# Kernel optimization log

Measured on AMD Instinct MI355X. Metric: run time of the kernel, lower is better.

Reference implementation:

```python
import jax, jax.numpy as jnp
import numpy as np

N_NODES = 50000
N_EDGES = 800000
D_IN = 64
D_HID = 64
N_LAYERS = 3
BN_EPS = 1e-5


def setup_inputs() -> dict:
    key = jax.random.key(0)
    ks = jax.random.split(key, 10)
    x = jax.random.normal(ks[0], (N_NODES, D_IN), dtype=jnp.float32)
    edge_index = jax.random.randint(ks[1], (2, N_EDGES), 0, N_NODES, dtype=jnp.int32)
    # Per-layer GCN weights (in==hid==64 so we can stack) and BatchNorm params.
    Ws = jax.random.normal(ks[2], (N_LAYERS, D_HID, D_HID), dtype=jnp.float32) / np.sqrt(D_HID)
    bs = jnp.zeros((N_LAYERS, D_HID), dtype=jnp.float32)
    gammas = jnp.ones((N_LAYERS, D_HID), dtype=jnp.float32)
    betas = jnp.zeros((N_LAYERS, D_HID), dtype=jnp.float32)
    means = jax.random.normal(ks[3], (N_LAYERS, D_HID), dtype=jnp.float32) * 0.1
    variances = jax.random.uniform(ks[4], (N_LAYERS, D_HID), dtype=jnp.float32, minval=0.5, maxval=1.5)
    lin_w = jax.random.normal(ks[5], (D_HID, 1), dtype=jnp.float32) / np.sqrt(D_HID)
    lin_b = jnp.zeros((1,), dtype=jnp.float32)
    return {"x": x, "edge_index": edge_index, "Ws": Ws, "bs": bs,
            "gammas": gammas, "betas": betas, "means": means,
            "variances": variances, "lin_w": lin_w, "lin_b": lin_b}


def _gnn_forward(x, edge_index, Ws, bs, gammas, betas, means, variances, lin_w, lin_b):
    n = x.shape[0]
    # GCNConv: add self loops, symmetric D^{-1/2}(A+I)D^{-1/2} normalization.
    loop = jnp.arange(n, dtype=edge_index.dtype)
    row = jnp.concatenate([edge_index[0], loop])  # source nodes
    col = jnp.concatenate([edge_index[1], loop])  # target nodes
    deg = jax.ops.segment_sum(jnp.ones(row.shape[0], x.dtype), col, num_segments=n)
    dinv = jax.lax.rsqrt(jnp.maximum(deg, 1.0))  # deg >= 1 from self loops
    norm = (dinv[row] * dinv[col])[:, None]  # [E+N, 1]

    h = x
    for i in range(N_LAYERS):
        h = h @ Ws[i]  # transform first (PyG GCNConv order)
        h = jax.ops.segment_sum(h[row] * norm, col, num_segments=n) + bs[i]
        # BatchNorm1d (eval mode: running stats) + ReLU; dropout is identity in eval.
        h = (h - means[i]) * jax.lax.rsqrt(variances[i] + BN_EPS) * gammas[i] + betas[i]
        h = jax.nn.relu(h)
    out = h @ lin_w + lin_b  # [N, 1]
    return out[:, 0]


def reference(x, edge_index, Ws, bs, gammas, betas, means, variances, lin_w, lin_b):
    return _gnn_forward(x, edge_index, Ws, bs, gammas, betas, means, variances, lin_w, lin_b)
```

## Files before the change

### kernel.cpp

```cpp
#include <hip/hip_runtime.h>
#include <hip/hip_bf16.h>
#include <hip/hip_fp16.h>


#define BN_EPS 1e-5f
#define CAP 64
#define CHUNK 2048
#define BINSH 7
#define SEGCAP 2560
#define NBINS_MAX 512

typedef _Float16 f16x8 __attribute__((ext_vector_type(8)));
typedef float f32x4 __attribute__((ext_vector_type(4)));

__global__ __launch_bounds__(256) void k_bin_pairs(const int* __restrict__ row,
                                                   const int* __restrict__ col,
                                                   int* __restrict__ gfill,
                                                   unsigned int* __restrict__ gpairs,
                                                   int e, int nbins) {
    __shared__ unsigned int pl[CHUNK];
    __shared__ int bcnt[NBINS_MAX];
    __shared__ int bbase[NBINS_MAX];
    int tid = threadIdx.x;
    int base = blockIdx.x * CHUNK;
    for (int b = tid; b < nbins; b += 256) bcnt[b] = 0;
    __syncthreads();
    int nloc = e - base; if (nloc > CHUNK) nloc = CHUNK;
    #pragma unroll
    for (int it = 0; it < CHUNK / 1024; ++it) {
        int le = (it * 256 + tid) * 4;
        if (le + 3 < nloc) {
            int i4 = (base >> 2) + it * 256 + tid;
            int4 r = ((const int4*)row)[i4];
            int4 c = ((const int4*)col)[i4];
            atomicAdd(&bcnt[c.x >> BINSH], 1); pl[le + 0] = (unsigned)r.x | ((unsigned)c.x << 16);
            atomicAdd(&bcnt[c.y >> BINSH], 1); pl[le + 1] = (unsigned)r.y | ((unsigned)c.y << 16);
            atomicAdd(&bcnt[c.z >> BINSH], 1); pl[le + 2] = (unsigned)r.z | ((unsigned)c.z << 16);
            atomicAdd(&bcnt[c.w >> BINSH], 1); pl[le + 3] = (unsigned)r.w | ((unsigned)c.w << 16);
        } else {
            for (int j = 0; j < 4; ++j) {
                if (le + j < nloc) {
                    int rr = row[base + le + j];
                    int cc = col[base + le + j];
                    atomicAdd(&bcnt[cc >> BINSH], 1);
                    pl[le + j] = (unsigned)rr | ((unsigned)cc << 16);
                }
            }
        }
    }
    __syncthreads();
    for (int b = tid; b < nbins; b += 256) {
        int cb = bcnt[b];
        bbase[b] = cb ? atomicAdd(&gfill[b], cb) : 0;
        bcnt[b] = 0;
    }
    __syncthreads();
    for (int i = tid; i < nloc; i += 256) {
        unsigned int p = pl[i];
        int bin = p >> (16 + BINSH);
        int off = atomicAdd(&bcnt[bin], 1);
        int pos = bbase[bin] + off;
        if (pos < SEGCAP) gpairs[(size_t)bin * SEGCAP + pos] = p;
    }
}

__global__ __launch_bounds__(256) void k_bucket_build(const unsigned int* __restrict__ gpairs,
                                                      const int* __restrict__ gfill,
                                                      int* __restrict__ cnt,
                                                      unsigned short* __restrict__ bucket,
                                                      const float* __restrict__ Ws,
                                                      __half* __restrict__ wt,
                                                      int n) {
    __shared__ unsigned short lb[128 * CAP];
    __shared__ int lc[128];
    int tid = threadIdx.x;
    int bin = blockIdx.x;
    if (tid < 128) lc[tid] = 0;
    __syncthreads();
    int m = gfill[bin]; if (m > SEGCAP) m = SEGCAP;
    const unsigned int* seg = gpairs + (size_t)bin * SEGCAP;
    for (int i = tid; i < m; i += 256) {
        unsigned int p = seg[i];
        int src = p & 0xffff;
        int dl = (p >> 16) & 127;
        int pos = atomicAdd(&lc[dl], 1);
        if (pos < CAP) lb[dl * CAP + pos] = (unsigned short)src;
    }
    __syncthreads();
    int nodebase = bin << BINSH;
    const int4* lb4 = (const int4*)lb;
    int4* gb4 = (int4*)bucket;
    for (int i = tid; i < 128 * 8; i += 256) {
        int rrow = i >> 3;
        int gnode = nodebase + rrow;
        if (gnode < n) gb4[(size_t)gnode * 8 + (i & 7)] = lb4[i];
    }
    if (tid < 128) {
        int gnode = nodebase + tid;
        if (gnode < n) cnt[gnode] = lc[tid];
    }
    if (bin < 3) {
        const float* W = Ws + bin * 4096;
        __half* hi = wt + (size_t)bin * 8192;
        __half* lo = hi + 4096;
        for (int i = tid; i < 4096; i += 256) {
            int k = i >> 6, nn = i & 63;
            float w = W[k * 64 + nn];
            __half h = __float2half_rn(w);
            hi[nn * 64 + k] = h;
            lo[nn * 64 + k] = __float2half_rn(w - __half2float(h));
        }
    }
}

template<bool L0>
__global__ __launch_bounds__(256) void k_mm_mfma(const void* __restrict__ Ain,
                                                 const __half* __restrict__ wt,
                                                 const int* __restrict__ cnt,
                                                 __half* __restrict__ out, int n) {
    int tid = threadIdx.x;
    int w = tid >> 6;
    int lane = tid & 63;
    int r = lane & 15;
    int kg = lane >> 4;
    int row = blockIdx.x * 64 + w * 16 + r;
    bool inb = row < n;

    f16x8 ahi0 = {}, ahi1 = {}, alo0 = {}, alo1 = {};
    if (L0) {
        const float* A = (const float*)Ain;
        if (inb) {
            float di = rsqrtf((float)(cnt[row] + 1));
            const float4* ap0 = (const float4*)(A + (size_t)row * 64 + kg * 8);
            const float4* ap1 = (const float4*)(A + (size_t)row * 64 + 32 + kg * 8);
            float4 v0 = ap0[0], v1 = ap0[1];
            float4 v2 = ap1[0], v3 = ap1[1];
            float f[16] = {v0.x, v0.y, v0.z, v0.w, v1.x, v1.y, v1.z, v1.w,
                           v2.x, v2.y, v2.z, v2.w, v3.x, v3.y, v3.z, v3.w};
            #pragma unroll
            for (int i = 0; i < 8; ++i) {
                float s0 = f[i] * di, s1 = f[8 + i] * di;
                _Float16 h0 = (_Float16)s0, h1 = (_Float16)s1;
                ahi0[i] = h0; ahi1[i] = h1;
                alo0[i] = (_Float16)(s0 - (float)h0);
                alo1[i] = (_Float16)(s1 - (float)h1);
            }
        }
    } else {
        const __half* A = (const __half*)Ain;
        if (inb) {
            union { uint4 u; f16x8 h; } u0, u1;
            u0.u = *(const uint4*)(A + (size_t)row * 64 + kg * 8);
            u1.u = *(const uint4*)(A + (size_t)row * 64 + 32 + kg * 8);
            ahi0 = u0.h; ahi1 = u1.h;
        }
    }

    const __half* whi = wt;
    const __half* wlo = wt + 4096;
    f32x4 acc[4];
    #pragma unroll
    for (int t = 0; t < 4; ++t) {
        int cb = t * 16 + r;
        union { uint4 u; f16x8 h; } bh0, bh1, bl0, bl1;
        bh0.u = *(const uint4*)(whi + cb * 64 + kg * 8);
        bh1.u = *(const uint4*)(whi + cb * 64 + 32 + kg * 8);
        bl0.u = *(const uint4*)(wlo + cb * 64 + kg * 8);
        bl1.u = *(const uint4*)(wlo + cb * 64 + 32 + kg * 8);
        f32x4 a = {0.f, 0.f, 0.f, 0.f};
        a = __builtin_amdgcn_mfma_f32_16x16x32_f16(ahi0, bh0.h, a, 0, 0, 0);
        a = __builtin_amdgcn_mfma_f32_16x16x32_f16(ahi1, bh1.h, a, 0, 0, 0);
        a = __builtin_amdgcn_mfma_f32_16x16x32_f16(ahi0, bl0.h, a, 0, 0, 0);
        a = __builtin_amdgcn_mfma_f32_16x16x32_f16(ahi1, bl1.h, a, 0, 0, 0);
        if (L0) {
            a = __builtin_amdgcn_mfma_f32_16x16x32_f16(alo0, bh0.h, a, 0, 0, 0);
            a = __builtin_amdgcn_mfma_f32_16x16x32_f16(alo1, bh1.h, a, 0, 0, 0);
        }
        acc[t] = a;
    }

    int orow_base = blockIdx.x * 64 + w * 16 + 4 * kg;
    #pragma unroll
    for (int t = 0; t < 4; ++t) {
        #pragma unroll
        for (int i = 0; i < 4; ++i) {
            int orow = orow_base + i;
            if (orow < n) out[(size_t)orow * 64 + t * 16 + r] = __float2half_rn(acc[t][i]);
        }
    }
}

template<int LAYER, bool FINAL>
__global__ __launch_bounds__(256, 6) void k_agg(const __half* __restrict__ t,
                                                const int* __restrict__ cnt,
                                                const unsigned short* __restrict__ bucket,
                                                const float* __restrict__ bias,
                                                const float* __restrict__ gamma,
                                                const float* __restrict__ beta,
                                                const float* __restrict__ mean,
                                                const float* __restrict__ var,
                                                __half* __restrict__ hout,
                                                const float* __restrict__ lw,
                                                const float* __restrict__ lb,
                                                float* __restrict__ outp, int n) {
    int lane = threadIdx.x & 63;
    int g = lane >> 3;
    int q = lane & 7;
    int qo = q << 3;
    float S[8], O[8], LW[8];
    #pragma unroll
    for (int i = 0; i < 8; ++i) {
        int f = qo + i;
        float s = gamma[f] * rsqrtf(var[f] + BN_EPS);
        S[i] = s;
        O[i] = fmaf(bias[f] - mean[f], s, beta[f]);
        if (FINAL) LW[i] = lw[f];
    }
    int wave = (blockIdx.x * blockDim.x + threadIdx.x) >> 6;
    int nwaves = (gridDim.x * blockDim.x) >> 6;
    union HV { float4 f4; __half2 h2[4]; };
    int node = wave;
    int c_pf = 0, idx_pf = 0;
    if (node < n) {
        c_pf = cnt[node];
        idx_pf = (int)bucket[(size_t)node * CAP + lane];
    }
    for (; node < n; node += nwaves) {
        int c = c_pf;
        int myidx = idx_pf;
        HV vself;
        vself.f4 = *(const float4*)(t + ((size_t)node << 6) + qo);
        int nn = node + nwaves;
        if (nn < n) {
            c_pf = cnt[nn];
            idx_pf = (int)bucket[(size_t)nn * CAP + lane];
        }
        int cm1 = c - 1; if (cm1 < 0) cm1 = 0;
        int i1 = __shfl(myidx, (g < cm1 ? g : cm1), 64);
        int i2 = __shfl(myidx, (8 + g < cm1 ? 8 + g : cm1), 64);
        HV v1, v2, v3, v4;
        v1.f4 = *(const float4*)(t + ((size_t)i1 << 6) + qo);
        v2.f4 = *(const float4*)(t + ((size_t)i2 << 6) + qo);
        if (c > 16) {
            int i3 = __shfl(myidx, (16 + g < cm1 ? 16 + g : cm1), 64);
            int i4 = __shfl(myidx, (24 + g < cm1 ? 24 + g : cm1), 64);
            v3.f4 = *(const float4*)(t + ((size_t)i3 << 6) + qo);
            v4.f4 = *(const float4*)(t + ((size_t)i4 << 6) + qo);
        }
        float acc[8] = {0.f, 0.f, 0.f, 0.f, 0.f, 0.f, 0.f, 0.f};
        for (int sub = 0; sub < c; sub += 32) {
            float m1 = (sub + g < c) ? 1.f : 0.f;
            float m2 = (sub + 8 + g < c) ? 1.f : 0.f;
            #pragma unroll
            for (int p = 0; p < 4; ++p) {
                float2 a = __half22float2(v1.h2[p]);
                float2 b = __half22float2(v2.h2[p]);
                acc[2 * p]     = fmaf(m1, a.x, acc[2 * p]);
                acc[2 * p + 1] = fmaf(m1, a.y, acc[2 * p + 1]);
                acc[2 * p]     = fmaf(m2, b.x, acc[2 * p]);
                acc[2 * p + 1] = fmaf(m2, b.y, acc[2 * p + 1]);
            }
            if (sub + 32 < c) {
                int t1 = sub + 32 + g, t2 = sub + 40 + g;
                i1 = __shfl(myidx, (t1 < cm1 ? t1 : cm1), 64);
                i2 = __shfl(myidx, (t2 < cm1 ? t2 : cm1), 64);
                v1.f4 = *(const float4*)(t + ((size_t)i1 << 6) + qo);
                v2.f4 = *(const float4*)(t + ((size_t)i2 << 6) + qo);
            }
            if (sub + 16 < c) {
                float m3 = (sub + 16 + g < c) ? 1.f : 0.f;
                float m4 = (sub + 24 + g < c) ? 1.f : 0.f;
                #pragma unroll
                for (int p = 0; p < 4; ++p) {
                    float2 a = __half22float2(v3.h2[p]);
                    float2 b = __half22float2(v4.h2[p]);
                    acc[2 * p]     = fmaf(m3, a.x, acc[2 * p]);
                    acc[2 * p + 1] = fmaf(m3, a.y, acc[2 * p + 1]);
                    acc[2 * p]     = fmaf(m4, b.x, acc[2 * p]);
                    acc[2 * p + 1] = fmaf(m4, b.y, acc[2 * p + 1]);
                }
            }
            if (sub + 48 < c) {
                int t3 = sub + 48 + g, t4 = sub + 56 + g;
                int i3 = __shfl(myidx, (t3 < cm1 ? t3 : cm1), 64);
                int i4 = __shfl(myidx, (t4 < cm1 ? t4 : cm1), 64);
                v3.f4 = *(const float4*)(t + ((size_t)i3 << 6) + qo);
                v4.f4 = *(const float4*)(t + ((size_t)i4 << 6) + qo);
            }
        }
        {
            float ms = (g == 0) ? 1.f : 0.f;
            #pragma unroll
            for (int p = 0; p < 4; ++p) {
                float2 a = __half22float2(vself.h2[p]);
                acc[2 * p]     = fmaf(ms, a.x, acc[2 * p]);
                acc[2 * p + 1] = fmaf(ms, a.y, acc[2 * p + 1]);
            }
        }
        #pragma unroll
        for (int i = 0; i < 8; ++i) {
            acc[i] += __shfl_down(acc[i], 32, 64);
            acc[i] += __shfl_down(acc[i], 16, 64);
            acc[i] += __shfl_down(acc[i], 8, 64);
        }
        float di = rsqrtf((float)(c + 1));
        if (FINAL) {
            float p = 0.f;
            #pragma unroll
            for (int i = 0; i < 8; ++i) {
                float h = fmaxf(fmaf(acc[i] * di, S[i], O[i]), 0.f);
                p = fmaf(h, LW[i], p);
            }
            p += __shfl_down(p, 4, 64);
            p += __shfl_down(p, 2, 64);
            p += __shfl_down(p, 1, 64);
            if (lane == 0) outp[node] = p + lb[0];
        } else if (g == 0) {
            union { __half2 h2[4]; uint4 u; } o;
            #pragma unroll
            for (int i = 0; i < 4; ++i) {
                float h0 = fmaxf(fmaf(acc[2 * i] * di, S[2 * i], O[2 * i]), 0.f);
                float h1 = fmaxf(fmaf(acc[2 * i + 1] * di, S[2 * i + 1], O[2 * i + 1]), 0.f);
                o.h2[i] = __floats2half2_rn(h0 * di, h1 * di);
            }
            *(uint4*)(hout + ((size_t)node << 6) + qo) = o.u;
        }
    }
}

extern "C" void kernel_launch(void* const* d_in, const int* in_sizes, int n_in,
                              void* d_out, int out_size, void* d_ws, size_t ws_size,
                              hipStream_t stream) {
    const float* x    = (const float*)d_in[0];
    const int*   ei   = (const int*)d_in[1];
    const float* Ws   = (const float*)d_in[2];
    const float* bs   = (const float*)d_in[3];
    const float* gam  = (const float*)d_in[4];
    const float* bet  = (const float*)d_in[5];
    const float* mean = (const float*)d_in[6];
    const float* var  = (const float*)d_in[7];
    const float* lw   = (const float*)d_in[8];
    const float* lb   = (const float*)d_in[9];
    float* out = (float*)d_out;

    const int n = in_sizes[0] / 64;
    const int e = in_sizes[1] / 2;
    const int* row = ei;
    const int* col = ei + e;
    const int nbins = (n + (1 << BINSH) - 1) >> BINSH;

    int* ws_i = (int*)d_ws;
    int* cnt = ws_i;
    int* gfill = ws_i + n;
    unsigned short* bucket = (unsigned short*)(ws_i + n + 512);
    __half* t16 = (__half*)(ws_i + n + 512 + 32 * (size_t)n);
    __half* h16 = t16 + 64 * (size_t)n;
    __half* wt = (__half*)(((uintptr_t)(h16 + 64 * (size_t)n) + 15) & ~(uintptr_t)15);
    unsigned int* gpairs = (unsigned int*)t16;

    int nb_p1 = (e + CHUNK - 1) / CHUNK;
    int nb_mm = (n + 63) / 64;
    int nb_ag = 1536;

    hipMemsetAsync(gfill, 0, NBINS_MAX * sizeof(int), stream);
    k_bin_pairs<<<nb_p1, 256, 0, stream>>>(row, col, gfill, gpairs, e, nbins);
    k_bucket_build<<<nbins, 256, 0, stream>>>(gpairs, gfill, cnt, bucket, Ws, wt, n);

    k_mm_mfma<true><<<nb_mm, 256, 0, stream>>>(x, wt, cnt, t16, n);
    k_agg<0, false><<<nb_ag, 256, 0, stream>>>(t16, cnt, bucket,
                                               bs, gam, bet, mean, var,
                                               h16, nullptr, nullptr, nullptr, n);
    k_mm_mfma<false><<<nb_mm, 256, 0, stream>>>(h16, wt + 8192, cnt, t16, n);
    k_agg<1, false><<<nb_ag, 256, 0, stream>>>(t16, cnt, bucket,
                                               bs + 64, gam + 64, bet + 64, mean + 64, var + 64,
                                               h16, nullptr, nullptr, nullptr, n);
    k_mm_mfma<false><<<nb_mm, 256, 0, stream>>>(h16, wt + 16384, cnt, t16, n);
    k_agg<2, true><<<nb_ag, 256, 0, stream>>>(t16, cnt, bucket,
                                              bs + 128, gam + 128, bet + 128, mean + 128, var + 128,
                                              nullptr, lw, lb, out, n);
}
```

Baseline: 257.6 us.

## Split feature matrix into two 32-column halves and aggregate each half separately

Stores the transformed node features as two planar halves of 32 columns each instead of one 64-wide row. The gather/aggregate kernel then makes two passes, one per half, so each neighbour gather touches 64 bytes and the working set per pass is halved. The intent is better cache hit rates for the random gathers. In exchange, the bucket and count reads are done twice, each index gather is issued twice, and the final output needs a read-modify-write across the two passes.

```diff
diff --git a/kernel.cpp b/kernel.cpp
--- a/kernel.cpp
+++ b/kernel.cpp
@@ -150,8 +150,8 @@
         const __half* A = (const __half*)Ain;
         if (inb) {
             union { uint4 u; f16x8 h; } u0, u1;
-            u0.u = *(const uint4*)(A + (size_t)row * 64 + kg * 8);
-            u1.u = *(const uint4*)(A + (size_t)row * 64 + 32 + kg * 8);
+            u0.u = *(const uint4*)(A + (size_t)row * 32 + kg * 8);
+            u1.u = *(const uint4*)(A + (size_t)n * 32 + (size_t)row * 32 + kg * 8);
             ahi0 = u0.h; ahi1 = u1.h;
         }
     }
@@ -182,10 +182,12 @@
     int orow_base = blockIdx.x * 64 + w * 16 + 4 * kg;
     #pragma unroll
     for (int t = 0; t < 4; ++t) {
+        int col = t * 16 + r;
+        __half* op = out + (size_t)(col >> 5) * 32 * n + (col & 31);
         #pragma unroll
         for (int i = 0; i < 4; ++i) {
             int orow = orow_base + i;
-            if (orow < n) out[(size_t)orow * 64 + t * 16 + r] = __float2half_rn(acc[t][i]);
+            if (orow < n) op[(size_t)orow * 32] = __float2half_rn(acc[t][i]);
         }
     }
 }
@@ -204,126 +206,118 @@
                                                 const float* __restrict__ lb,
                                                 float* __restrict__ outp, int n) {
     int lane = threadIdx.x & 63;
-    int g = lane >> 3;
-    int q = lane & 7;
+    int g = lane >> 2;
+    int q = lane & 3;
     int qo = q << 3;
-    float S[8], O[8], LW[8];
-    #pragma unroll
-    for (int i = 0; i < 8; ++i) {
-        int f = qo + i;
-        float s = gamma[f] * rsqrtf(var[f] + BN_EPS);
-        S[i] = s;
-        O[i] = fmaf(bias[f] - mean[f], s, beta[f]);
-        if (FINAL) LW[i] = lw[f];
-    }
     int wave = (blockIdx.x * blockDim.x + threadIdx.x) >> 6;
     int nwaves = (gridDim.x * blockDim.x) >> 6;
     union HV { float4 f4; __half2 h2[4]; };
-    int node = wave;
-    int c_pf = 0, idx_pf = 0;
-    if (node < n) {
-        c_pf = cnt[node];
-        idx_pf = (int)bucket[(size_t)node * CAP + lane];
-    }
-    for (; node < n; node += nwaves) {
-        int c = c_pf;
-        int myidx = idx_pf;
-        HV vself;
-        vself.f4 = *(const float4*)(t + ((size_t)node << 6) + qo);
-        int nn = node + nwaves;
-        if (nn < n) {
-            c_pf = cnt[nn];
-            idx_pf = (int)bucket[(size_t)nn * CAP + lane];
-        }
-        int cm1 = c - 1; if (cm1 < 0) cm1 = 0;
-        int i1 = __shfl(myidx, (g < cm1 ? g : cm1), 64);
-        int i2 = __shfl(myidx, (8 + g < cm1 ? 8 + g : cm1), 64);
-        HV v1, v2, v3, v4;
-        v1.f4 = *(const float4*)(t + ((size_t)i1 << 6) + qo);
-        v2.f4 = *(const float4*)(t + ((size_t)i2 << 6) + qo);
-        if (c > 16) {
-            int i3 = __shfl(myidx, (16 + g < cm1 ? 16 + g : cm1), 64);
-            int i4 = __shfl(myidx, (24 + g < cm1 ? 24 + g : cm1), 64);
-            v3.f4 = *(const float4*)(t + ((size_t)i3 << 6) + qo);
-            v4.f4 = *(const float4*)(t + ((size_t)i4 << 6) + qo);
-        }
-        float acc[8] = {0.f, 0.f, 0.f, 0.f, 0.f, 0.f, 0.f, 0.f};
-        for (int sub = 0; sub < c; sub += 32) {
-            float m1 = (sub + g < c) ? 1.f : 0.f;
-            float m2 = (sub + 8 + g < c) ? 1.f : 0.f;
-            #pragma unroll
-            for (int p = 0; p < 4; ++p) {
-                float2 a = __half22float2(v1.h2[p]);
-                float2 b = __half22float2(v2.h2[p]);
-                acc[2 * p]     = fmaf(m1, a.x, acc[2 * p]);
-                acc[2 * p + 1] = fmaf(m1, a.y, acc[2 * p + 1]);
-                acc[2 * p]     = fmaf(m2, b.x, acc[2 * p]);
-                acc[2 * p + 1] = fmaf(m2, b.y, acc[2 * p + 1]);
-            }
-            if (sub + 32 < c) {
-                int t1 = sub + 32 + g, t2 = sub + 40 + g;
-                i1 = __shfl(myidx, (t1 < cm1 ? t1 : cm1), 64);
-                i2 = __shfl(myidx, (t2 < cm1 ? t2 : cm1), 64);
-                v1.f4 = *(const float4*)(t + ((size_t)i1 << 6) + qo);
-                v2.f4 = *(const float4*)(t + ((size_t)i2 << 6) + qo);
-            }
-            if (sub + 16 < c) {
-                float m3 = (sub + 16 + g < c) ? 1.f : 0.f;
-                float m4 = (sub + 24 + g < c) ? 1.f : 0.f;
+    for (int ph = 0; ph < 2; ++ph) {
+        const __half* tp = t + (size_t)ph * 32 * n;
+        __half* hp = hout + (size_t)ph * 32 * n;
+        float S[8], O[8], LW[8];
+        #pragma unroll
+        for (int i = 0; i < 8; ++i) {
+            int f = ph * 32 + qo + i;
+            float s = gamma[f] * rsqrtf(var[f] + BN_EPS);
+            S[i] = s;
+            O[i] = fmaf(bias[f] - mean[f], s, beta[f]);
+            if (FINAL) LW[i] = lw[f];
+        }
+        int node = wave;
+        int c_pf = 0, idx_pf = 0;
+        if (node < n) {
+            c_pf = cnt[node];
+            idx_pf = (int)bucket[(size_t)node * CAP + lane];
+        }
+        for (; node < n; node += nwaves) {
+            int c = c_pf;
+            int myidx = idx_pf;
+            HV vself;
+            vself.f4 = *(const float4*)(tp + ((size_t)node << 5) + qo);
+            int nn = node + nwaves;
+            if (nn < n) {
+                c_pf = cnt[nn];
+                idx_pf = (int)bucket[(size_t)nn * CAP + lane];
+            }
+            int cm1 = c - 1; if (cm1 < 0) cm1 = 0;
+            int i1 = __shfl(myidx, (g < cm1 ? g : cm1), 64);
+            HV v1, v2;
+            v1.f4 = *(const float4*)(tp + ((size_t)i1 << 5) + qo);
+            if (c > 16) {
+                int i2 = __shfl(myidx, (16 + g < cm1 ? 16 + g : cm1), 64);
+                v2.f4 = *(const float4*)(tp + ((size_t)i2 << 5) + qo);
+            }
+            float acc[8] = {0.f, 0.f, 0.f, 0.f, 0.f, 0.f, 0.f, 0.f};
+            for (int sub = 0; sub < c; sub += 32) {
+                float m1 = (sub + g < c) ? 1.f : 0.f;
+                HV u1 = v1, u2 = v2;
+                if (sub + 32 < c) {
+                    int t1 = sub + 32 + g;
+                    i1 = __shfl(myidx, (t1 < cm1 ? t1 : cm1), 64);
+                    v1.f4 = *(const float4*)(tp + ((size_t)i1 << 5) + qo);
+                }
+                if (sub + 48 < c) {
+                    int t2 = sub + 48 + g;
+                    int i2 = __shfl(myidx, (t2 < cm1 ? t2 : cm1), 64);
+                    v2.f4 = *(const float4*)(tp + ((size_t)i2 << 5) + qo);
+                }
                 #pragma unroll
                 for (int p = 0; p < 4; ++p) {
-                    float2 a = __half22float2(v3.h2[p]);
-                    float2 b = __half22float2(v4.h2[p]);
-                    acc[2 * p]     = fmaf(m3, a.x, acc[2 * p]);
-                    acc[2 * p + 1] = fmaf(m3, a.y, acc[2 * p + 1]);
-                    acc[2 * p]     = fmaf(m4, b.x, acc[2 * p]);
-                    acc[2 * p + 1] = fmaf(m4, b.y, acc[2 * p + 1]);
-                }
-            }
-            if (sub + 48 < c) {
-                int t3 = sub + 48 + g, t4 = sub + 56 + g;
-                int i3 = __shfl(myidx, (t3 < cm1 ? t3 : cm1), 64);
-                int i4 = __shfl(myidx, (t4 < cm1 ? t4 : cm1), 64);
-                v3.f4 = *(const float4*)(t + ((size_t)i3 << 6) + qo);
-                v4.f4 = *(const float4*)(t + ((size_t)i4 << 6) + qo);
-            }
-        }
-        {
-            float ms = (g == 0) ? 1.f : 0.f;
-            #pragma unroll
-            for (int p = 0; p < 4; ++p) {
-                float2 a = __half22float2(vself.h2[p]);
-                acc[2 * p]     = fmaf(ms, a.x, acc[2 * p]);
-                acc[2 * p + 1] = fmaf(ms, a.y, acc[2 * p + 1]);
-            }
-        }
-        #pragma unroll
-        for (int i = 0; i < 8; ++i) {
-            acc[i] += __shfl_down(acc[i], 32, 64);
-            acc[i] += __shfl_down(acc[i], 16, 64);
-            acc[i] += __shfl_down(acc[i], 8, 64);
-        }
-        float di = rsqrtf((float)(c + 1));
-        if (FINAL) {
-            float p = 0.f;
+                    float2 a = __half22float2(u1.h2[p]);
+                    acc[2 * p]     = fmaf(m1, a.x, acc[2 * p]);
+                    acc[2 * p + 1] = fmaf(m1, a.y, acc[2 * p + 1]);
+                }
+                if (sub + 16 < c) {
+                    float m2 = (sub + 16 + g < c) ? 1.f : 0.f;
+                    #pragma unroll
+                    for (int p = 0; p < 4; ++p) {
+                        float2 b = __half22float2(u2.h2[p]);
+                        acc[2 * p]     = fmaf(m2, b.x, acc[2 * p]);
+                        acc[2 * p + 1] = fmaf(m2, b.y, acc[2 * p + 1]);
+                    }
+                }
+            }
+            {
+                float ms = (g == 0) ? 1.f : 0.f;
+                #pragma unroll
+                for (int p = 0; p < 4; ++p) {
+                    float2 a = __half22float2(vself.h2[p]);
+                    acc[2 * p]     = fmaf(ms, a.x, acc[2 * p]);
+                    acc[2 * p + 1] = fmaf(ms, a.y, acc[2 * p + 1]);
+                }
+            }
             #pragma unroll
             for (int i = 0; i < 8; ++i) {
-                float h = fmaxf(fmaf(acc[i] * di, S[i], O[i]), 0.f);
-                p = fmaf(h, LW[i], p);
-            }
-            p += __shfl_down(p, 4, 64);
-            p += __shfl_down(p, 2, 64);
-            p += __shfl_down(p, 1, 64);
-            if (lane == 0) outp[node] = p + lb[0];
-        } else if (g == 0) {
-            union { __half2 h2[4]; uint4 u; } o;
-            #pragma unroll
-            for (int i = 0; i < 4; ++i) {
-                float h0 = fmaxf(fmaf(acc[2 * i] * di, S[2 * i], O[2 * i]), 0.f);
-                float h1 = fmaxf(fmaf(acc[2 * i + 1] * di, S[2 * i + 1], O[2 * i + 1]), 0.f);
-                o.h2[i] = __floats2half2_rn(h0 * di, h1 * di);
-            }
-            *(uint4*)(hout + ((size_t)node << 6) + qo) = o.u;
+                acc[i] += __shfl_down(acc[i], 32, 64);
+                acc[i] += __shfl_down(acc[i], 16, 64);
+                acc[i] += __shfl_down(acc[i], 8, 64);
+                acc[i] += __shfl_down(acc[i], 4, 64);
+            }
+            float di = rsqrtf((float)(c + 1));
+            if (FINAL) {
+                float p = 0.f;
+                #pragma unroll
+                for (int i = 0; i < 8; ++i) {
+                    float h = fmaxf(fmaf(acc[i] * di, S[i], O[i]), 0.f);
+                    p = fmaf(h, LW[i], p);
+                }
+                p += __shfl_down(p, 2, 64);
+                p += __shfl_down(p, 1, 64);
+                if (lane == 0) {
+                    if (ph == 0) outp[node] = p;
+                    else         outp[node] = outp[node] + p + lb[0];
+                }
+            } else if (g == 0) {
+                union { __half2 h2[4]; uint4 u; } o;
+                #pragma unroll
+                for (int i = 0; i < 4; ++i) {
+                    float h0 = fmaxf(fmaf(acc[2 * i] * di, S[2 * i], O[2 * i]), 0.f);
+                    float h1 = fmaxf(fmaf(acc[2 * i + 1] * di, S[2 * i + 1], O[2 * i + 1]), 0.f);
+                    o.h2[i] = __floats2half2_rn(h0 * di, h1 * di);
+                }
+                *(uint4*)(hp + ((size_t)node << 5) + qo) = o.u;
+            }
         }
     }
 }
```

Result: slower. 296.6 us (+15.1%).
